# Performance work log

Hardware: AMD Instinct MI355X
Metric: run time of the kernel (lower is better)

## Reference

```python
import jax, jax.numpy as jnp
import numpy as np

HIDDEN = 512
HEADS = 8
HEAD_DIM = HIDDEN // HEADS  # 64
NUM_FEATURES = 256
EPS = 1e-4


def _gaussian_orthogonal_random_matrix(num_rows, num_cols, scaling=0, seed=1234):
    """Blocks of orthogonal rows from QR of gaussian matrices, rescaled (FAVOR+)."""
    rng = np.random.default_rng(seed)
    blocks = []
    full_blocks = num_rows // num_cols
    for _ in range(full_blocks):
        q, _ = np.linalg.qr(rng.standard_normal((num_cols, num_cols)))
        blocks.append(q.T)
    rem = num_rows - full_blocks * num_cols
    if rem > 0:
        q, _ = np.linalg.qr(rng.standard_normal((num_cols, num_cols)))
        blocks.append(q.T[:rem])
    mat = np.concatenate(blocks, axis=0)  # [num_rows, num_cols]
    if scaling == 0:
        # row norms of a fresh gaussian matrix (chi-distributed multipliers)
        multiplier = np.linalg.norm(rng.standard_normal((num_rows, num_cols)), axis=1)
    else:
        multiplier = np.sqrt(num_cols) * np.ones(num_rows)
    return (multiplier[:, None] * mat).astype(np.float32)


def _split_heads(x, b):
    # [b, n, hidden] -> [b, h, n, head_dim]
    return x.reshape(b, -1, HEADS, HEAD_DIM).transpose(0, 2, 1, 3)


def _phi(data, proj):
    """Nonnegative softmax kernel feature map (FAVOR+).
    data: [b,h,n,d], proj: [m,d] -> [b,h,n,m]"""
    d = data.shape[-1]
    m = proj.shape[0]
    x = data * (d ** -0.25)
    dash = jnp.einsum('bhnd,md->bhnm', x, proj)
    diag = 0.5 * jnp.sum(x * x, axis=-1, keepdims=True)
    return (m ** -0.5) * jnp.exp(dash - diag) + EPS


def setup_inputs() -> dict:
    key = jax.random.key(0)
    ks = jax.random.split(key, 12)
    b, n = 2, 8192
    s = HIDDEN ** -0.5
    inp = {
        'query': jax.random.normal(ks[0], (b, n, HIDDEN), jnp.float32),
        'key':   jax.random.normal(ks[1], (b, n, HIDDEN), jnp.float32),
        'value': jax.random.normal(ks[2], (b, n, HIDDEN), jnp.float32),
        'WQ_w': jax.random.normal(ks[3], (HIDDEN, HIDDEN), jnp.float32) * s,
        'WQ_b': jnp.zeros((HIDDEN,), jnp.float32),
        'WK_w': jax.random.normal(ks[4], (HIDDEN, HIDDEN), jnp.float32) * s,
        'WK_b': jnp.zeros((HIDDEN,), jnp.float32),
        'WV_w': jax.random.normal(ks[5], (HIDDEN, HIDDEN), jnp.float32) * s,
        'WV_b': jnp.zeros((HIDDEN,), jnp.float32),
        'WO_w': jax.random.normal(ks[6], (HIDDEN, HIDDEN), jnp.float32) * s,
        'WO_b': jnp.zeros((HIDDEN,), jnp.float32),
        'proj': jnp.asarray(_gaussian_orthogonal_random_matrix(NUM_FEATURES, HEAD_DIM)),
    }
    return inp


def reference(query, key, value, WQ_w, WQ_b, WK_w, WK_b, WV_w, WV_b, WO_w, WO_b, proj):
    b = query.shape[0]
    # torch Linear: y = x @ W.T + b
    Q = _split_heads(jnp.einsum('bnd,ed->bne', query, WQ_w) + WQ_b, b)
    K = _split_heads(jnp.einsum('bnd,ed->bne', key,   WK_w) + WK_b, b)
    V = _split_heads(jnp.einsum('bnd,ed->bne', value, WV_w) + WV_b, b)

    Qp = _phi(Q, proj)  # [b,h,n,m]
    Kp = _phi(K, proj)  # [b,h,n,m]

    # denominator: Q' @ sum_n K'  -> [b,h,n,1]
    denom = jnp.einsum('bhnm,bhm->bhn', Qp, jnp.sum(Kp, axis=2))[..., None]
    # linear attention: Q' @ (K'^T V), O(n*m*d)
    ctx = jnp.einsum('bhnm,bhnd->bhmd', Kp, V)
    attn = jnp.einsum('bhnm,bhmd->bhnd', Qp, ctx) / denom

    # faithful to original: .view(batch, -1, hidden) directly on [b,h,n,d]
    attn = attn.reshape(b, -1, HIDDEN)
    return jnp.einsum('bnd,ed->bne', attn, WO_w) + WO_b
```

## Files before the change

kernel.cpp:

```cpp
#include <hip/hip_runtime.h>

typedef __attribute__((ext_vector_type(8))) _Float16 f16x8;
typedef __attribute__((ext_vector_type(4))) float f32x4;

#define S4 0.35355339059327373f

static __device__ __forceinline__ ushort f2h(float f) {
  return __builtin_bit_cast(ushort, (_Float16)f);
}

static __device__ __forceinline__ void gload16(const void* g, void* l) {
  __builtin_amdgcn_global_load_lds((const __attribute__((address_space(1))) void*)g,
                                   (__attribute__((address_space(3))) void*)l, 16, 0, 0);
}

static __device__ __forceinline__ void cvt_store8(ushort* dst, float4 a, float4 b) {
  f16x8 h;
  h[0] = (_Float16)a.x; h[1] = (_Float16)a.y; h[2] = (_Float16)a.z; h[3] = (_Float16)a.w;
  h[4] = (_Float16)b.x; h[5] = (_Float16)b.y; h[6] = (_Float16)b.z; h[7] = (_Float16)b.w;
  *(f16x8*)dst = h;
}

template<int BM, int BN, int WR, int WC, int EPI, int ZMODE, int DIAG, int AF32, int BF32>
__global__ __launch_bounds__(256) void gemm_bt(
    const void* __restrict__ Av, const void* __restrict__ Bv,
    const float* __restrict__ bias, ushort* __restrict__ Cb,
    float* __restrict__ Cf, const float* __restrict__ rv0,
    float* __restrict__ dg,
    int K, int ldA, int ldB, int ldC, int Mz,
    long sAz, long sBz, long sCz)
{
  constexpr int BK = 32;
  constexpr int WTM = BM / WR, WTN = BN / WC;
  constexpr int MI = WTM / 16, NI = WTN / 16;
  constexpr int LDSB = (BM + BN) * 64;

  __shared__ uint4 smem4[LDSB / 16];
  char* smem = (char*)smem4;
  ushort* As = (ushort*)smem;
  ushort* Bs = (ushort*)(smem + BM * 64);

  const int tid = threadIdx.x;
  const int l = tid & 63, w = tid >> 6;
  const int wr = w / WC, wc = w % WC;
  const int lr = l & 15, lk = l >> 4;
  const int tm = blockIdx.x * BM, tn = blockIdx.y * BN;
  const int z = blockIdx.z;

  const ushort* Ah = (const ushort*)Av;
  const ushort* Bh = (const ushort*)Bv;
  const float*  Af = (const float*)Av;
  const float*  Bf = (const float*)Bv;
  long aoff = 0, boff = 0;
  if (ZMODE == 0) { aoff = (long)z * sAz; boff = (long)z * sBz; }
  if (ZMODE == 2) { aoff = (long)z * sAz; boff = (long)(z >> 3) * sBz + (z & 7) * 64; }
  if (ZMODE == 3) {
    aoff = (long)(z & 15) * sAz + (long)(z >> 4) * 1024;
    boff = (long)(z & 15) * sBz + (long)(z >> 4) * 1024;
  }
  Ah += aoff; Bh += boff; Af += aoff; Bf += boff;
  const float* rv = (EPI == 6) ? (rv0 + (long)z * Mz) : nullptr;
  const long coff = (long)z * sCz;

  f32x4 acc[MI][NI];
#pragma unroll
  for (int i = 0; i < MI; ++i)
#pragma unroll
    for (int j = 0; j < NI; ++j) acc[i][j] = f32x4{0.f, 0.f, 0.f, 0.f};

  for (int k0 = 0; k0 < K; k0 += BK) {
    if constexpr (AF32) {
      const int ar = tid >> 1, ac = (tid & 1) * 16;
      const float* g = Af + (long)(tm + ar) * ldA + k0 + ac;
      float4 f0 = *(const float4*)(g);
      float4 f1 = *(const float4*)(g + 4);
      float4 f2 = *(const float4*)(g + 8);
      float4 f3 = *(const float4*)(g + 12);
      cvt_store8(As + ar * 32 + ac, f0, f1);
      cvt_store8(As + ar * 32 + ac + 8, f2, f3);
    } else {
      constexpr int AB = BM * 64;
#pragma unroll
      for (int s = 0; s < (AB + 4095) / 4096; ++s) {
        const int base = s * 4096 + w * 1024;
        if (base < AB) {
          const int idx = base + l * 16;
          gload16(Ah + (long)(tm + (idx >> 6)) * ldA + k0 + ((idx & 63) >> 1),
                  (char*)As + base);
        }
      }
    }
    if constexpr (BF32) {
      const int br = tid >> 1, bc = (tid & 1) * 16;
      const float* g = Bf + (long)(tn + br) * ldB + k0 + bc;
      float4 f0 = *(const float4*)(g);
      float4 f1 = *(const float4*)(g + 4);
      float4 f2 = *(const float4*)(g + 8);
      float4 f3 = *(const float4*)(g + 12);
      cvt_store8(Bs + br * 32 + bc, f0, f1);
      cvt_store8(Bs + br * 32 + bc + 8, f2, f3);
    } else {
      constexpr int BB = BN * 64;
#pragma unroll
      for (int s = 0; s < (BB + 4095) / 4096; ++s) {
        const int base = s * 4096 + w * 1024;
        if (base < BB) {
          const int idx = base + l * 16;
          gload16(Bh + (long)(tn + (idx >> 6)) * ldB + k0 + ((idx & 63) >> 1),
                  (char*)Bs + base);
        }
      }
    }
    __syncthreads();

    f16x8 af[MI], bfr[NI];
#pragma unroll
    for (int mi = 0; mi < MI; ++mi)
      af[mi] = *(const f16x8*)(As + (wr * WTM + mi * 16 + lr) * 32 + lk * 8);
#pragma unroll
    for (int ni = 0; ni < NI; ++ni)
      bfr[ni] = *(const f16x8*)(Bs + (wc * WTN + ni * 16 + lr) * 32 + lk * 8);
#pragma unroll
    for (int mi = 0; mi < MI; ++mi)
#pragma unroll
      for (int ni = 0; ni < NI; ++ni)
        acc[mi][ni] = __builtin_amdgcn_mfma_f32_16x16x32_f16(af[mi], bfr[ni], acc[mi][ni], 0, 0, 0);
    __syncthreads();
  }

#pragma unroll
  for (int mi = 0; mi < MI; ++mi) {
#pragma unroll
    for (int j = 0; j < 4; ++j) {
      const int row = tm + wr * WTM + mi * 16 + lk * 4 + j;
      float ds = 0.f;
#pragma unroll
      for (int ni = 0; ni < NI; ++ni) {
        const int col = tn + wc * WTN + ni * 16 + lr;
        float v = acc[mi][ni][j];
        if (EPI == 0 || EPI == 3) v += bias[col];
        if (EPI == 4) v += bias[row];
        if (EPI == 6) v = 0.0625f * __expf(v - rv[col]) + 1e-4f;
        if (DIAG) ds += v * v;
        if (EPI == 4) {
          const int b = col >> 13, nn = col & 8191;
          const int h = row >> 6, d = row & 63;
          Cb[(long)(b * 8 + h) * 655360 + (long)d * 8192 + nn] = f2h(v);
        } else if (EPI == 3 || EPI == 5) {
          Cf[coff + (long)row * ldC + col] = v;
        } else {
          Cb[coff + (long)row * ldC + col] = f2h(v);
        }
      }
      if (DIAG) {
        ds += __shfl_xor(ds, 1, 64);
        ds += __shfl_xor(ds, 2, 64);
        ds += __shfl_xor(ds, 4, 64);
        ds += __shfl_xor(ds, 8, 64);
        if (lr == 0) {
          const int b = row >> 13, nn = row & 8191;
          const int head = (tn + wc * WTN) >> 6;
          dg[(long)(b * 8 + head) * 8192 + nn] = 0.0625f * ds;
        }
      }
    }
  }
}

__global__ __launch_bounds__(256) void phiattn_k(
    const ushort* __restrict__ Qh, const ushort* __restrict__ pjh,
    const float* __restrict__ diagQ, const ushort* __restrict__ ctxb,
    ushort* __restrict__ attnR)
{
  const int bx = blockIdx.x, bh = blockIdx.y;
  const int b = bh >> 3, h = bh & 7;
  const int tm = bx * 128;
  const int tid = threadIdx.x, l = tid & 63, w = tid >> 6;
  const int lr = l & 15, lk = l >> 4;
  const int wr = w >> 1, wc = w & 1;

  __shared__ char smem[126208];
  ushort* P  = (ushort*)smem;
  ushort* Cs = (ushort*)(smem + 67584);
  ushort* As = (ushort*)(smem + 109824);
  ushort* Bs = (ushort*)(smem + 118016);

  {
    const ushort* cb = ctxb + (long)bh * 20480;
#pragma unroll
    for (int c = tid; c < 2560; c += 256) {
      const int row = c >> 5, cole = (c & 31) * 8;
      *(uint4*)(Cs + row * 264 + cole) = *(const uint4*)(cb + row * 256 + cole);
    }
  }
  const ushort* QB = Qh + (long)b * 4194304 + h * 64;
  const float* rv = diagQ + (long)bh * 8192;

  for (int nh = 0; nh < 2; ++nh) {
    const ushort* PB = pjh + nh * 8192;
    f32x4 a2[4][4];
#pragma unroll
    for (int i = 0; i < 4; ++i)
#pragma unroll
      for (int j = 0; j < 4; ++j) a2[i][j] = f32x4{0.f, 0.f, 0.f, 0.f};

    for (int k0 = 0; k0 < 64; k0 += 32) {
#pragma unroll
      for (int s = 0; s < 2; ++s) {
        const int base = s * 4096 + w * 1024;
        const int idx = base + l * 16;
        gload16(QB + (long)(tm + (idx >> 6)) * 512 + k0 + ((idx & 63) >> 1),
                (char*)As + base);
      }
#pragma unroll
      for (int s = 0; s < 2; ++s) {
        const int base = s * 4096 + w * 1024;
        const int idx = base + l * 16;
        gload16(PB + (long)(idx >> 6) * 64 + k0 + ((idx & 63) >> 1),
                (char*)Bs + base);
      }
      __syncthreads();
      f16x8 af[4], bfr[4];
#pragma unroll
      for (int mi = 0; mi < 4; ++mi)
        af[mi] = *(const f16x8*)(As + (wr * 64 + mi * 16 + lr) * 32 + lk * 8);
#pragma unroll
      for (int ni = 0; ni < 4; ++ni)
        bfr[ni] = *(const f16x8*)(Bs + (wc * 64 + ni * 16 + lr) * 32 + lk * 8);
#pragma unroll
      for (int mi = 0; mi < 4; ++mi)
#pragma unroll
        for (int ni = 0; ni < 4; ++ni)
          a2[mi][ni] = __builtin_amdgcn_mfma_f32_16x16x32_f16(af[mi], bfr[ni], a2[mi][ni], 0, 0, 0);
      __syncthreads();
    }
#pragma unroll
    for (int mi = 0; mi < 4; ++mi)
#pragma unroll
      for (int ni = 0; ni < 4; ++ni)
#pragma unroll
        for (int j = 0; j < 4; ++j) {
          const int row = wr * 64 + mi * 16 + lk * 4 + j;
          const int col = nh * 128 + wc * 64 + ni * 16 + lr;
          const float vv = 0.0625f * __expf(a2[mi][ni][j] - rv[tm + row]) + 1e-4f;
          P[row * 264 + col] = f2h(vv);
        }
  }
  __syncthreads();

  f32x4 acc[2][5];
#pragma unroll
  for (int i = 0; i < 2; ++i)
#pragma unroll
    for (int j = 0; j < 5; ++j) acc[i][j] = f32x4{0.f, 0.f, 0.f, 0.f};

  for (int k0 = 0; k0 < 256; k0 += 32) {
    f16x8 pa[2], cbf[5];
#pragma unroll
    for (int mi = 0; mi < 2; ++mi)
      pa[mi] = *(const f16x8*)(P + (w * 32 + mi * 16 + lr) * 264 + k0 + lk * 8);
#pragma unroll
    for (int ni = 0; ni < 5; ++ni)
      cbf[ni] = *(const f16x8*)(Cs + (ni * 16 + lr) * 264 + k0 + lk * 8);
#pragma unroll
    for (int mi = 0; mi < 2; ++mi)
#pragma unroll
      for (int ni = 0; ni < 5; ++ni)
        acc[mi][ni] = __builtin_amdgcn_mfma_f32_16x16x32_f16(pa[mi], cbf[ni], acc[mi][ni], 0, 0, 0);
  }

  ushort* outb = attnR + (long)bh * 524288;
#pragma unroll
  for (int mi = 0; mi < 2; ++mi)
#pragma unroll
    for (int j = 0; j < 4; ++j) {
      const float dv = __shfl(acc[mi][4][j], (l & 48), 64);
      const int row = tm + w * 32 + mi * 16 + lk * 4 + j;
#pragma unroll
      for (int ni = 0; ni < 4; ++ni) {
        const int col = ni * 16 + lr;
        outb[(long)row * 64 + col] = f2h(acc[mi][ni][j] / dv);
      }
    }
}

__global__ __launch_bounds__(256) void cvtall_k(
    const float* __restrict__ wq, const float* __restrict__ wk,
    const float* __restrict__ wv, const float* __restrict__ wo,
    const float* __restrict__ pj,
    ushort* __restrict__ wqh, ushort* __restrict__ wkh,
    ushort* __restrict__ wvh, ushort* __restrict__ woh,
    ushort* __restrict__ pjh)
{
  int i = blockIdx.x * 256 + threadIdx.x;
  const float* in; ushort* out; float scale = 1.f; int idx;
  if (i < 65536)       { in = wq; out = wqh; idx = i; }
  else if (i < 131072) { in = wk; out = wkh; idx = i - 65536; }
  else if (i < 196608) { in = wv; out = wvh; idx = i - 131072; }
  else if (i < 262144) { in = wo; out = woh; idx = i - 196608; }
  else if (i < 266240) { in = pj; out = pjh; idx = i - 262144; scale = S4; }
  else return;
  float4 v = ((const float4*)in)[idx];
  ushort4 o;
  o.x = f2h(v.x * scale); o.y = f2h(v.y * scale);
  o.z = f2h(v.z * scale); o.w = f2h(v.w * scale);
  ((ushort4*)out)[idx] = o;
}

__global__ __launch_bounds__(256) void vtpad_k(ushort* __restrict__ Vt) {
  const int i = blockIdx.x * 256 + threadIdx.x;
  const int bh = i >> 14, rem = i & 16383, r = rem >> 10, n8 = rem & 1023;
  const unsigned val = (r == 0) ? 0x3C003C00u : 0u;
  uint4 u; u.x = val; u.y = val; u.z = val; u.w = val;
  *(uint4*)(Vt + (long)bh * 655360 + (long)(64 + r) * 8192 + n8 * 8) = u;
}

__global__ __launch_bounds__(256) void ctxred_k(const float* __restrict__ cp,
                                                ushort* __restrict__ ctxb) {
  const int idx = blockIdx.x * 256 + threadIdx.x;
  const int bh = idx / 20480, rem = idx % 20480;
  float a = 0.f;
#pragma unroll
  for (int kc = 0; kc < 8; ++kc) a += cp[(long)(kc * 16 + bh) * 20480 + rem];
  ctxb[idx] = f2h(a);
}

extern "C" void kernel_launch(void* const* d_in, const int* in_sizes, int n_in,
                              void* d_out, int out_size, void* d_ws, size_t ws_size,
                              hipStream_t stream) {
  (void)in_sizes; (void)n_in; (void)out_size; (void)ws_size;
  const float* q  = (const float*)d_in[0];
  const float* k  = (const float*)d_in[1];
  const float* v  = (const float*)d_in[2];
  const float* wq = (const float*)d_in[3];
  const float* bq = (const float*)d_in[4];
  const float* wk = (const float*)d_in[5];
  const float* bk = (const float*)d_in[6];
  const float* wv = (const float*)d_in[7];
  const float* bv = (const float*)d_in[8];
  const float* wo = (const float*)d_in[9];
  const float* bo = (const float*)d_in[10];
  const float* pj = (const float*)d_in[11];

  char* ws = (char*)d_ws;
  ushort* attnR = (ushort*)(ws + 0);
  float*  cpart = (float*)(ws + 16777216);
  ushort* wqh   = (ushort*)(ws + 27262976);
  ushort* wkh   = (ushort*)(ws + 27787264);
  ushort* wvh   = (ushort*)(ws + 28311552);
  ushort* woh   = (ushort*)(ws + 28835840);
  ushort* pjh   = (ushort*)(ws + 29360128);
  ushort* Qh    = (ushort*)(ws + 29392896);
  ushort* Kh    = (ushort*)(ws + 46170112);
  ushort* Vt    = (ushort*)(ws + 62947328);
  ushort* KpT   = (ushort*)(ws + 83918848);
  float*  diagQ = (float*)(ws + 151027712);
  float*  diagK = (float*)(ws + 151552000);
  ushort* ctxb  = (ushort*)(ws + 152076288);

  cvtall_k<<<1040, 256, 0, stream>>>(wq, wk, wv, wo, pj, wqh, wkh, wvh, woh, pjh);
  vtpad_k<<<1024, 256, 0, stream>>>(Vt);

  gemm_bt<128,128,2,2,0,0,1,1,0><<<dim3(128,4,1), 256, 0, stream>>>(
      q, wqh, bq, Qh, nullptr, nullptr, diagQ, 512, 512, 512, 512, 0, 0L, 0L, 0L);
  gemm_bt<128,128,2,2,0,0,1,1,0><<<dim3(128,4,1), 256, 0, stream>>>(
      k, wkh, bk, Kh, nullptr, nullptr, diagK, 512, 512, 512, 512, 0, 0L, 0L, 0L);

  gemm_bt<128,128,2,2,4,0,0,0,1><<<dim3(4,128,1), 256, 0, stream>>>(
      wvh, v, bv, Vt, nullptr, nullptr, nullptr, 512, 512, 512, 0, 0, 0L, 0L, 0L);

  gemm_bt<128,128,2,2,6,2,0,0,0><<<dim3(2,64,16), 256, 0, stream>>>(
      pjh, Kh, nullptr, KpT, nullptr, diagK, nullptr, 64, 64, 512, 8192, 8192,
      0L, 4194304L, 2097152L);

  gemm_bt<80,128,1,4,5,3,0,0,0><<<dim3(1,2,128), 256, 0, stream>>>(
      Vt, KpT, nullptr, nullptr, cpart, nullptr, nullptr, 1024, 8192, 8192, 256, 0,
      655360L, 2097152L, 20480L);
  ctxred_k<<<1280, 256, 0, stream>>>(cpart, ctxb);

  phiattn_k<<<dim3(64,16), 256, 0, stream>>>(Qh, pjh, diagQ, ctxb, attnR);

  gemm_bt<128,128,2,2,3,0,0,0,0><<<dim3(128,4,1), 256, 0, stream>>>(
      attnR, woh, bo, nullptr, (float*)d_out, nullptr, nullptr, 512, 512, 512, 512, 0,
      0L, 0L, 0L);
}
```

Baseline: 201.8 us.

## Halve phiattn row tile and read ctx fragments directly from global

The phi+attention kernel now processes 64 query rows per block instead of 128, with each wave owning 16 rows across all 128 feature columns, and launches twice as many blocks. The ctx matrix is no longer staged in LDS; MFMA B fragments are loaded straight from global memory (L2-cached). Shared memory drops from about 126KB to 46KB, which allows more resident blocks per CU and better latency hiding. The cost is more redundant global/L2 reads of ctx and the projection matrix, plus lower MFMA reuse per loaded fragment.

```diff
diff --git a/kernel.cpp b/kernel.cpp
--- a/kernel.cpp
+++ b/kernel.cpp
@@ -174,40 +174,27 @@
 {
   const int bx = blockIdx.x, bh = blockIdx.y;
   const int b = bh >> 3, h = bh & 7;
-  const int tm = bx * 128;
+  const int tm = bx * 64;
   const int tid = threadIdx.x, l = tid & 63, w = tid >> 6;
   const int lr = l & 15, lk = l >> 4;
-  const int wr = w >> 1, wc = w & 1;
-
-  __shared__ char smem[126208];
+
+  __shared__ char smem[46080];
   ushort* P  = (ushort*)smem;
-  ushort* Cs = (ushort*)(smem + 67584);
-  ushort* As = (ushort*)(smem + 109824);
-  ushort* Bs = (ushort*)(smem + 118016);
-
-  {
-    const ushort* cb = ctxb + (long)bh * 20480;
-#pragma unroll
-    for (int c = tid; c < 2560; c += 256) {
-      const int row = c >> 5, cole = (c & 31) * 8;
-      *(uint4*)(Cs + row * 264 + cole) = *(const uint4*)(cb + row * 256 + cole);
-    }
-  }
+  ushort* As = (ushort*)(smem + 33792);
+  ushort* Bs = (ushort*)(smem + 37888);
+
   const ushort* QB = Qh + (long)b * 4194304 + h * 64;
   const float* rv = diagQ + (long)bh * 8192;
 
   for (int nh = 0; nh < 2; ++nh) {
     const ushort* PB = pjh + nh * 8192;
-    f32x4 a2[4][4];
-#pragma unroll
-    for (int i = 0; i < 4; ++i)
-#pragma unroll
-      for (int j = 0; j < 4; ++j) a2[i][j] = f32x4{0.f, 0.f, 0.f, 0.f};
+    f32x4 a2[8];
+#pragma unroll
+    for (int i = 0; i < 8; ++i) a2[i] = f32x4{0.f, 0.f, 0.f, 0.f};
 
     for (int k0 = 0; k0 < 64; k0 += 32) {
-#pragma unroll
-      for (int s = 0; s < 2; ++s) {
-        const int base = s * 4096 + w * 1024;
+      {
+        const int base = w * 1024;
         const int idx = base + l * 16;
         gload16(QB + (long)(tm + (idx >> 6)) * 512 + k0 + ((idx & 63) >> 1),
                 (char*)As + base);
@@ -220,68 +207,51 @@
                 (char*)Bs + base);
       }
       __syncthreads();
-      f16x8 af[4], bfr[4];
-#pragma unroll
-      for (int mi = 0; mi < 4; ++mi)
-        af[mi] = *(const f16x8*)(As + (wr * 64 + mi * 16 + lr) * 32 + lk * 8);
-#pragma unroll
-      for (int ni = 0; ni < 4; ++ni)
-        bfr[ni] = *(const f16x8*)(Bs + (wc * 64 + ni * 16 + lr) * 32 + lk * 8);
-#pragma unroll
-      for (int mi = 0; mi < 4; ++mi)
-#pragma unroll
-        for (int ni = 0; ni < 4; ++ni)
-          a2[mi][ni] = __builtin_amdgcn_mfma_f32_16x16x32_f16(af[mi], bfr[ni], a2[mi][ni], 0, 0, 0);
+      f16x8 af = *(const f16x8*)(As + (w * 16 + lr) * 32 + lk * 8);
+#pragma unroll
+      for (int ni = 0; ni < 8; ++ni) {
+        f16x8 bfr = *(const f16x8*)(Bs + (ni * 16 + lr) * 32 + lk * 8);
+        a2[ni] = __builtin_amdgcn_mfma_f32_16x16x32_f16(af, bfr, a2[ni], 0, 0, 0);
+      }
       __syncthreads();
     }
 #pragma unroll
-    for (int mi = 0; mi < 4; ++mi)
-#pragma unroll
-      for (int ni = 0; ni < 4; ++ni)
-#pragma unroll
-        for (int j = 0; j < 4; ++j) {
-          const int row = wr * 64 + mi * 16 + lk * 4 + j;
-          const int col = nh * 128 + wc * 64 + ni * 16 + lr;
-          const float vv = 0.0625f * __expf(a2[mi][ni][j] - rv[tm + row]) + 1e-4f;
-          P[row * 264 + col] = f2h(vv);
-        }
+    for (int ni = 0; ni < 8; ++ni)
+#pragma unroll
+      for (int j = 0; j < 4; ++j) {
+        const int row = w * 16 + lk * 4 + j;
+        const int col = nh * 128 + ni * 16 + lr;
+        const float vv = 0.0625f * __expf(a2[ni][j] - rv[tm + row]) + 1e-4f;
+        P[row * 264 + col] = f2h(vv);
+      }
   }
   __syncthreads();
 
-  f32x4 acc[2][5];
-#pragma unroll
-  for (int i = 0; i < 2; ++i)
-#pragma unroll
-    for (int j = 0; j < 5; ++j) acc[i][j] = f32x4{0.f, 0.f, 0.f, 0.f};
-
+  f32x4 acc[5];
+#pragma unroll
+  for (int i = 0; i < 5; ++i) acc[i] = f32x4{0.f, 0.f, 0.f, 0.f};
+
+  const ushort* cb = ctxb + (long)bh * 20480;
   for (int k0 = 0; k0 < 256; k0 += 32) {
-    f16x8 pa[2], cbf[5];
-#pragma unroll
-    for (int mi = 0; mi < 2; ++mi)
-      pa[mi] = *(const f16x8*)(P + (w * 32 + mi * 16 + lr) * 264 + k0 + lk * 8);
-#pragma unroll
-    for (int ni = 0; ni < 5; ++ni)
-      cbf[ni] = *(const f16x8*)(Cs + (ni * 16 + lr) * 264 + k0 + lk * 8);
-#pragma unroll
-    for (int mi = 0; mi < 2; ++mi)
-#pragma unroll
-      for (int ni = 0; ni < 5; ++ni)
-        acc[mi][ni] = __builtin_amdgcn_mfma_f32_16x16x32_f16(pa[mi], cbf[ni], acc[mi][ni], 0, 0, 0);
+    f16x8 pa = *(const f16x8*)(P + (w * 16 + lr) * 264 + k0 + lk * 8);
+#pragma unroll
+    for (int ni = 0; ni < 5; ++ni) {
+      f16x8 cf = *(const f16x8*)(cb + (long)(ni * 16 + lr) * 256 + k0 + lk * 8);
+      acc[ni] = __builtin_amdgcn_mfma_f32_16x16x32_f16(pa, cf, acc[ni], 0, 0, 0);
+    }
   }
 
   ushort* outb = attnR + (long)bh * 524288;
 #pragma unroll
-  for (int mi = 0; mi < 2; ++mi)
-#pragma unroll
-    for (int j = 0; j < 4; ++j) {
-      const float dv = __shfl(acc[mi][4][j], (l & 48), 64);
-      const int row = tm + w * 32 + mi * 16 + lk * 4 + j;
-#pragma unroll
-      for (int ni = 0; ni < 4; ++ni) {
-        const int col = ni * 16 + lr;
-        outb[(long)row * 64 + col] = f2h(acc[mi][ni][j] / dv);
-      }
-    }
+  for (int j = 0; j < 4; ++j) {
+    const float dv = __shfl(acc[4][j], (l & 48), 64);
+    const int row = tm + w * 16 + lk * 4 + j;
+#pragma unroll
+    for (int ni = 0; ni < 4; ++ni) {
+      const int col = ni * 16 + lr;
+      outb[(long)row * 64 + col] = f2h(acc[ni][j] / dv);
+    }
+  }
 }
 
 __global__ __launch_bounds__(256) void cvtall_k(
@@ -378,7 +348,7 @@
       655360L, 2097152L, 20480L);
   ctxred_k<<<1280, 256, 0, stream>>>(cpart, ctxb);
 
-  phiattn_k<<<dim3(64,16), 256, 0, stream>>>(Qh, pjh, diagQ, ctxb, attnR);
+  phiattn_k<<<dim3(128,16), 256, 0, stream>>>(Qh, pjh, diagQ, ctxb, attnR);
 
   gemm_bt<128,128,2,2,3,0,0,0,0><<<dim3(128,4,1), 256, 0, stream>>>(
       attnR, woh, bo, nullptr, (float*)d_out, nullptr, nullptr, 512, 512, 512, 512, 0,
```

Result: slower. 210.9 us (+4.5%).
